# Optimization experiments

Measured on AMD Instinct MI355X. Metric: run time of the kernel, lower is better.

## Reference

```python
import jax, jax.numpy as jnp
import numpy as np

NUM_HEADS = 32
HEAD_DIM = 128
HIDDEN = NUM_HEADS * HEAD_DIM  # 4096
ROPE_BASE = 10000.0
VISION_TOKEN_TYPE = 1


def vision_expert_mask(token_type_ids):
    # vision_token_mask[:, :-1] = (tt[:, :-1]==1) & (tt[:, 1:]==1); last col False
    tt = token_type_ids
    m = (tt[:, :-1] == VISION_TOKEN_TYPE) & (tt[:, 1:] == VISION_TOKEN_TYPE)
    return jnp.concatenate([m, jnp.zeros((tt.shape[0], 1), dtype=bool)], axis=1)


def rotary_cos_sin(position_ids, head_dim, dtype):
    inv_freq = 1.0 / (ROPE_BASE ** (jnp.arange(0, head_dim, 2, dtype=jnp.float32) / head_dim))
    freqs = position_ids.astype(jnp.float32)[..., None] * inv_freq  # [B,S,Dh/2]
    emb = jnp.concatenate([freqs, freqs], axis=-1)  # [B,S,Dh]
    return jnp.cos(emb).astype(dtype), jnp.sin(emb).astype(dtype)


def rotate_half(x):
    d = x.shape[-1] // 2
    return jnp.concatenate([-x[..., d:], x[..., :d]], axis=-1)


def setup_inputs() -> dict:
    key = jax.random.key(0)
    ks = jax.random.split(key, 5)
    B, S = 2, 2048
    hidden_states = jax.random.normal(ks[0], (B, S, HIDDEN), dtype=jnp.float32)
    token_type_ids = jax.random.randint(ks[1], (B, S), 0, 2, dtype=jnp.int64)
    position_ids = jnp.broadcast_to(jnp.arange(S, dtype=jnp.int64)[None, :], (B, S))
    scale = 0.02
    w_vis_qkv = jax.random.normal(ks[2], (HIDDEN, 3 * HIDDEN), dtype=jnp.float32) * scale
    w_lang_qkv = jax.random.normal(ks[3], (HIDDEN, 3 * HIDDEN), dtype=jnp.float32) * scale
    w_vis_dense = jax.random.normal(ks[4], (HIDDEN, HIDDEN), dtype=jnp.float32) * scale
    w_lang_dense = jax.random.normal(jax.random.fold_in(key, 7), (HIDDEN, HIDDEN), dtype=jnp.float32) * scale
    return dict(hidden_states=hidden_states, token_type_ids=token_type_ids,
                position_ids=position_ids, w_vis_qkv=w_vis_qkv, w_lang_qkv=w_lang_qkv,
                w_vis_dense=w_vis_dense, w_lang_dense=w_lang_dense)


def reference(hidden_states, token_type_ids, position_ids,
              w_vis_qkv, w_lang_qkv, w_vis_dense, w_lang_dense):
    B, S, D = hidden_states.shape
    vm = vision_expert_mask(token_type_ids)  # [B,S] bool

    # 2-expert QKV dispatch (mask-select between the two expert GEMMs)
    qkv = jnp.where(vm[..., None],
                    hidden_states @ w_vis_qkv,
                    hidden_states @ w_lang_qkv)  # [B,S,3D]
    q, k, v = jnp.split(qkv, 3, axis=-1)
    q = q.reshape(B, S, NUM_HEADS, HEAD_DIM)
    k = k.reshape(B, S, NUM_HEADS, HEAD_DIM)
    v = v.reshape(B, S, NUM_HEADS, HEAD_DIM)

    # rotary embedding on q, k
    cos, sin = rotary_cos_sin(position_ids, HEAD_DIM, q.dtype)  # [B,S,Dh]
    cos, sin = cos[:, :, None, :], sin[:, :, None, :]
    q = q * cos + rotate_half(q) * sin
    k = k * cos + rotate_half(k) * sin

    # causal attention (dense equivalent of the paged-attention call)
    scores = jnp.einsum('bqhd,bkhd->bhqk', q, k) / jnp.sqrt(jnp.array(HEAD_DIM, q.dtype))
    causal = jnp.tril(jnp.ones((S, S), dtype=bool))
    scores = jnp.where(causal[None, None], scores, jnp.finfo(scores.dtype).min)
    probs = jax.nn.softmax(scores, axis=-1)
    ctx = jnp.einsum('bhqk,bkhd->bqhd', probs, v).reshape(B, S, D)

    # 2-expert output dense dispatch
    attn_output = jnp.where(vm[..., None],
                            ctx @ w_vis_dense,
                            ctx @ w_lang_dense)
    return attn_output
```

## Files before the change

kernel.cpp:

```cpp
#include <hip/hip_runtime.h>
#include <math.h>

#define SEQ     2048
#define NB      2
#define NHEADS  32
#define DHEAD   128
#define HID     4096
#define NQKV    12288
#define T_TOKENS (NB*SEQ)

typedef _Float16 half8 __attribute__((ext_vector_type(8)));
typedef float v4f __attribute__((ext_vector_type(4)));

__device__ __forceinline__ void gload_lds16(const void* g, void* l) {
    __builtin_amdgcn_global_load_lds(
        (__attribute__((address_space(1))) void*)(void*)(g),
        (__attribute__((address_space(3))) void*)(unsigned)(unsigned long long)(l),
        16, 0, 0);
}

__device__ __forceinline__ v4f mfma16(half8 a, half8 b, v4f c) {
    return __builtin_amdgcn_mfma_f32_16x16x32_f16(a, b, c, 0, 0, 0);
}

__global__ void route_kernel(const int* __restrict__ tt, int* counts, int* idx) {
    int t = blockIdx.x * blockDim.x + threadIdx.x;
    if (t >= T_TOKENS) return;
    int s = t & (SEQ - 1);
    bool vm = (s < SEQ - 1) && (tt[t] == 1) && (tt[t + 1] == 1);
    int e = vm ? 0 : 1;
    int p = atomicAdd(&counts[e], 1);
    idx[e * T_TOKENS + p] = t;
}

__global__ void rope_table_kernel(const int* __restrict__ pos_ids, float2* __restrict__ tab) {
    int i = blockIdx.x * blockDim.x + threadIdx.x;
    if (i >= T_TOKENS * 64) return;
    int tok = i >> 6, j = i & 63;
    float invf = (float)pow(10000.0, -(double)j * (1.0 / 64.0));
    float ang = (float)pos_ids[tok] * invf;
    double ds, dc;
    sincos((double)ang, &ds, &dc);
    tab[i] = make_float2((float)dc, (float)ds);
}

__global__ void cvt_f32_f16(const float* __restrict__ src, _Float16* __restrict__ dst, int n4) {
    int i = blockIdx.x * blockDim.x + threadIdx.x;
    if (i >= n4) return;
    float4 v = ((const float4*)src)[i];
    union { _Float16 h[4]; uint2 u; } p;
    p.h[0] = (_Float16)v.x; p.h[1] = (_Float16)v.y;
    p.h[2] = (_Float16)v.z; p.h[3] = (_Float16)v.w;
    ((uint2*)dst)[i] = p.u;
}

__global__ void transpose_cvt(const float* __restrict__ W, _Float16* __restrict__ WT,
                              int K, int N) {
    __shared__ _Float16 t[64][72];
    const int n0 = blockIdx.x * 64, k0 = blockIdx.y * 64;
    const int cr = threadIdx.x & 15, rr = threadIdx.x >> 4;
#pragma unroll
    for (int it = 0; it < 4; ++it) {
        int r = rr + it * 16;
        float4 v = *(const float4*)&W[(size_t)(k0 + r) * N + n0 + cr * 4];
        t[cr*4+0][r] = (_Float16)v.x; t[cr*4+1][r] = (_Float16)v.y;
        t[cr*4+2][r] = (_Float16)v.z; t[cr*4+3][r] = (_Float16)v.w;
    }
    __syncthreads();
#pragma unroll
    for (int it = 0; it < 4; ++it) {
        int r = rr + it * 16;
        union { _Float16 h[4]; uint2 u; } p;
#pragma unroll
        for (int j = 0; j < 4; ++j) p.h[j] = t[r][cr*4+j];
        *(uint2*)&WT[(size_t)(n0 + r) * K + k0 + cr * 4] = p.u;
    }
}

__global__ void transpose_v(const _Float16* __restrict__ vin, _Float16* __restrict__ vout) {
    __shared__ _Float16 t[64][72];
    const int s0 = blockIdx.x * 64;
    const int d0 = blockIdx.y * 64;
    const int bh = blockIdx.z;
    const int b = bh >> 5, h = bh & 31;
    const int cr = threadIdx.x & 15, rr = threadIdx.x >> 4;
#pragma unroll
    for (int it = 0; it < 4; ++it) {
        int sl = rr + it * 16;
        union { _Float16 h4[4]; uint2 u; } p;
        p.u = *(const uint2*)&vin[(size_t)(b * SEQ + s0 + sl) * HID + h * DHEAD + d0 + cr * 4];
#pragma unroll
        for (int j = 0; j < 4; ++j) t[cr*4+j][sl] = p.h4[j];
    }
    __syncthreads();
#pragma unroll
    for (int it = 0; it < 4; ++it) {
        int dl = rr + it * 16;
        union { _Float16 h4[4]; uint2 u; } p;
#pragma unroll
        for (int j = 0; j < 4; ++j) p.h4[j] = t[dl][cr*4+j];
        *(uint2*)&vout[((size_t)bh * DHEAD + d0 + dl) * SEQ + s0 + cr * 4] = p.u;
    }
}

template <int MODE, int NCT>
__global__ __launch_bounds__(256, 2)
void gemm_expert(const _Float16* __restrict__ A,
                 const _Float16* __restrict__ BT0,
                 const _Float16* __restrict__ BT1,
                 const int* __restrict__ counts,
                 const int* __restrict__ idx_all,
                 const float2* __restrict__ rope,
                 _Float16* __restrict__ qbuf,
                 _Float16* __restrict__ kbuf,
                 _Float16* __restrict__ vbuf,
                 float* __restrict__ out) {
    const int e = blockIdx.z;
    const int count = counts[e];

    const int f   = blockIdx.x + NCT * blockIdx.y;
    const int xcd = f & 7;
    const int g   = f >> 3;
    const int c   = g >> 6;
    const int wi  = g & 63;
    const int rt  = wi >> 1;
    const int ct  = xcd * (NCT / 8) + c * 2 + (wi & 1);

    if (rt * 128 >= count) return;
    const int* idx = idx_all + e * T_TOKENS;
    const _Float16* BT = e ? BT1 : BT0;

    __shared__ _Float16 sA[2][128 * 32];
    __shared__ _Float16 sB[2][128 * 32];

    const int tid = threadIdx.x;
    const int w = tid >> 6, lane = tid & 63;
    const int col = lane & 15, quad = lane >> 4;

    const int r0 = (w * 2 + 0) * 16 + (lane >> 2);
    const int r1 = (w * 2 + 1) * 16 + (lane >> 2);
    int g0 = rt * 128 + r0; if (g0 > count - 1) g0 = count - 1;
    int g1 = rt * 128 + r1; if (g1 > count - 1) g1 = count - 1;
    const int tok0 = idx[g0], tok1 = idx[g1];
    const _Float16* ag0 = A + (size_t)tok0 * HID + (lane & 3) * 8;
    const _Float16* ag1 = A + (size_t)tok1 * HID + (lane & 3) * 8;
    const _Float16* bg0 = BT + (size_t)(ct * 128 + r0) * HID + (lane & 3) * 8;
    const _Float16* bg1 = BT + (size_t)(ct * 128 + r1) * HID + (lane & 3) * 8;
    const int sa_off0 = (w * 2 + 0) * 512;
    const int sa_off1 = (w * 2 + 1) * 512;

    v4f acc[2][8];
#pragma unroll
    for (int i = 0; i < 2; ++i)
#pragma unroll
        for (int j = 0; j < 8; ++j) { v4f z = {0.f, 0.f, 0.f, 0.f}; acc[i][j] = z; }

    const int am0 = (w * 32 + col) * 32 + quad * 8;
    const int am1 = am0 + 16 * 32;

    gload_lds16(ag0, &sA[0][sa_off0]); gload_lds16(ag1, &sA[0][sa_off1]);
    gload_lds16(bg0, &sB[0][sa_off0]); gload_lds16(bg1, &sB[0][sa_off1]);
    ag0 += 32; ag1 += 32; bg0 += 32; bg1 += 32;
    __syncthreads();

    for (int kt = 0; kt < HID / 32; ++kt) {
        const int cur = kt & 1, nxt = cur ^ 1;
        if (kt + 1 < HID / 32) {
            gload_lds16(ag0, &sA[nxt][sa_off0]); gload_lds16(ag1, &sA[nxt][sa_off1]);
            gload_lds16(bg0, &sB[nxt][sa_off0]); gload_lds16(bg1, &sB[nxt][sa_off1]);
            ag0 += 32; ag1 += 32; bg0 += 32; bg1 += 32;
        }
        half8 a0 = *(const half8*)&sA[cur][am0];
        half8 a1 = *(const half8*)&sA[cur][am1];
#pragma unroll
        for (int nt = 0; nt < 8; ++nt) {
            half8 b = *(const half8*)&sB[cur][(nt * 16 + col) * 32 + quad * 8];
            acc[0][nt] = mfma16(a0, b, acc[0][nt]);
            acc[1][nt] = mfma16(a1, b, acc[1][nt]);
        }
        __syncthreads();
    }

    const int n0 = ct * 128;
    if (MODE == 1) {
#pragma unroll
        for (int mt = 0; mt < 2; ++mt)
#pragma unroll
            for (int r = 0; r < 4; ++r) {
                int rg = rt * 128 + w * 32 + mt * 16 + quad * 4 + r;
                if (rg >= count) continue;
                int tok = idx[rg];
                float* dst = out + (size_t)tok * HID + n0;
#pragma unroll
                for (int nt = 0; nt < 8; ++nt) dst[nt * 16 + col] = acc[mt][nt][r];
            }
    } else {
        const int sec = n0 >> 12;
        const int h = (n0 >> 7) & 31;
#pragma unroll
        for (int mt = 0; mt < 2; ++mt)
#pragma unroll
            for (int r = 0; r < 4; ++r) {
                int rg = rt * 128 + w * 32 + mt * 16 + quad * 4 + r;
                if (rg >= count) continue;
                int tok = idx[rg];
                int b = tok >> 11, s = tok & (SEQ - 1);
                if (sec == 2) {
                    _Float16* dst = vbuf + (size_t)tok * HID + h * DHEAD;
#pragma unroll
                    for (int nt = 0; nt < 8; ++nt) dst[nt * 16 + col] = (_Float16)acc[mt][nt][r];
                } else {
                    _Float16* dst = (sec ? kbuf : qbuf) + ((size_t)(b * NHEADS + h) * SEQ + s) * DHEAD;
                    const float2* tp = rope + (size_t)tok * 64;
#pragma unroll
                    for (int nt = 0; nt < 4; ++nt) {
                        int d = nt * 16 + col;
                        float2 cs = tp[d];
                        float x = acc[mt][nt][r], y = acc[mt][nt + 4][r];
                        dst[d]      = (_Float16)(x * cs.x - y * cs.y);
                        dst[d + 64] = (_Float16)(y * cs.x + x * cs.y);
                    }
                }
            }
    }
}

__global__ __launch_bounds__(256, 2)
void attn_kernel(const _Float16* __restrict__ qbuf,
                 const _Float16* __restrict__ kbuf,
                 const _Float16* __restrict__ vt,
                 _Float16* __restrict__ ctx) {
    const int f   = blockIdx.x;
    const int xcd = f & 7;
    const int t   = f >> 3;
    const int s   = t & 31;
    const int rr  = t >> 5;
    const int u   = s & 15, g = s >> 4;
    const int bh  = xcd * 8 + rr * 2 + g;
    const int qt  = (rr & 1) ? (15 - u) : u;

    const int b = bh >> 5, h = bh & 31;
    const int tid = threadIdx.x;
    const int w = tid >> 6, lane = tid & 63;
    const int col = lane & 15, quad = lane >> 4;

    __shared__ _Float16 sK[2][64 * 128];
    __shared__ _Float16 sV[2][128 * 64];
    __shared__ _Float16 sP[128 * 64];

    half8 qf[2][4];
    const _Float16 qscale = (_Float16)0.08838834764831845f;
#pragma unroll
    for (int mt = 0; mt < 2; ++mt)
#pragma unroll
        for (int kc = 0; kc < 4; ++kc) {
            int row = qt * 128 + w * 32 + mt * 16 + col;
            half8 v = *(const half8*)&qbuf[((size_t)bh * SEQ + row) * DHEAD + kc * 32 + quad * 8];
            qf[mt][kc] = v * qscale;
        }

    float mrow[2][4], lrow[2][4];
    v4f o[2][8];
#pragma unroll
    for (int mt = 0; mt < 2; ++mt)
#pragma unroll
        for (int r = 0; r < 4; ++r) { mrow[mt][r] = -3.0e38f; lrow[mt][r] = 0.f; }
#pragma unroll
    for (int i = 0; i < 2; ++i)
#pragma unroll
        for (int j = 0; j < 8; ++j) { v4f z = {0.f, 0.f, 0.f, 0.f}; o[i][j] = z; }

    const int cxor = col & 7;
    const int vs_chk = (lane & 7) ^ (lane >> 3);
    const int nkt = 2 * qt + 2;

    const _Float16* kg0 = kbuf + (size_t)bh * SEQ * DHEAD;
    const _Float16* vg0 = vt + (size_t)bh * DHEAD * SEQ;

    auto stage = [&](int kt, int buf) {
        const _Float16* kg = kg0 + (size_t)kt * 64 * DHEAD;
        const _Float16* vg = vg0 + kt * 64;
#pragma unroll
        for (int op = 0; op < 4; ++op) {
            int r0 = (w * 4 + op) * 4;
            int krow = r0 + quad;
            int kcs = col ^ (krow & 7);
            gload_lds16(kg + (size_t)krow * DHEAD + kcs * 8, &sK[buf][r0 * 128]);
            int d0 = (w * 4 + op) * 8;
            int vrow = d0 + (lane >> 3);
            gload_lds16(vg + (size_t)vrow * SEQ + vs_chk * 8, &sV[buf][d0 * 64]);
        }
    };

    stage(0, 0);
    __syncthreads();

    for (int kt = 0; kt < nkt; ++kt) {
        const int cur = kt & 1;
        if (kt + 1 < nkt) stage(kt + 1, cur ^ 1);

        v4f sc[2][4];
#pragma unroll
        for (int i = 0; i < 2; ++i)
#pragma unroll
            for (int j = 0; j < 4; ++j) { v4f z = {0.f, 0.f, 0.f, 0.f}; sc[i][j] = z; }
#pragma unroll
        for (int kc = 0; kc < 4; ++kc) {
            const int kof = ((kc * 4 + quad) ^ cxor) * 8;
#pragma unroll
            for (int nt = 0; nt < 4; ++nt) {
                half8 bf = *(const half8*)&sK[cur][(size_t)(nt * 16 + col) * 128 + kof];
                sc[0][nt] = mfma16(qf[0][kc], bf, sc[0][nt]);
                sc[1][nt] = mfma16(qf[1][kc], bf, sc[1][nt]);
            }
        }

        if (kt >= 2 * qt) {
#pragma unroll
            for (int mt = 0; mt < 2; ++mt)
#pragma unroll
                for (int nt = 0; nt < 4; ++nt)
#pragma unroll
                    for (int r = 0; r < 4; ++r) {
                        int rowa = qt * 128 + w * 32 + mt * 16 + quad * 4 + r;
                        int cola = kt * 64 + nt * 16 + col;
                        if (cola > rowa) sc[mt][nt][r] = -3.0e38f;
                    }
        }

#pragma unroll
        for (int mt = 0; mt < 2; ++mt)
#pragma unroll
            for (int r = 0; r < 4; ++r) {
                float mx = sc[mt][0][r];
#pragma unroll
                for (int nt = 1; nt < 4; ++nt) mx = fmaxf(mx, sc[mt][nt][r]);
                mx = fmaxf(mx, __shfl_xor(mx, 1));
                mx = fmaxf(mx, __shfl_xor(mx, 2));
                mx = fmaxf(mx, __shfl_xor(mx, 4));
                mx = fmaxf(mx, __shfl_xor(mx, 8));
                float newm = fmaxf(mrow[mt][r], mx);
                float alpha = __expf(mrow[mt][r] - newm);
                mrow[mt][r] = newm;
                float rs = 0.f;
#pragma unroll
                for (int nt = 0; nt < 4; ++nt) {
                    float p = __expf(sc[mt][nt][r] - newm);
                    sc[mt][nt][r] = p;
                    rs += p;
                }
                rs += __shfl_xor(rs, 1); rs += __shfl_xor(rs, 2);
                rs += __shfl_xor(rs, 4); rs += __shfl_xor(rs, 8);
                lrow[mt][r] = lrow[mt][r] * alpha + rs;
#pragma unroll
                for (int nt = 0; nt < 8; ++nt) o[mt][nt][r] *= alpha;
            }

#pragma unroll
        for (int mt = 0; mt < 2; ++mt)
#pragma unroll
            for (int nt = 0; nt < 4; ++nt)
#pragma unroll
                for (int r = 0; r < 4; ++r) {
                    int rp = w * 32 + mt * 16 + quad * 4 + r;
                    int colh = nt * 16 + col;
                    int c = (colh >> 3) ^ (rp & 7);
                    sP[(size_t)rp * 64 + c * 8 + (colh & 7)] = (_Float16)sc[mt][nt][r];
                }

#pragma unroll
        for (int kc = 0; kc < 2; ++kc) {
            const int kof = ((kc * 4 + quad) ^ cxor) * 8;
            half8 p0 = *(const half8*)&sP[(size_t)(w * 32 + col) * 64 + kof];
            half8 p1 = *(const half8*)&sP[(size_t)(w * 32 + 16 + col) * 64 + kof];
#pragma unroll
            for (int nt = 0; nt < 8; ++nt) {
                half8 vf = *(const half8*)&sV[cur][(size_t)(nt * 16 + col) * 64 + kof];
                o[0][nt] = mfma16(p0, vf, o[0][nt]);
                o[1][nt] = mfma16(p1, vf, o[1][nt]);
            }
        }

        __syncthreads();
    }

#pragma unroll
    for (int mt = 0; mt < 2; ++mt)
#pragma unroll
        for (int r = 0; r < 4; ++r) {
            int rowa = qt * 128 + w * 32 + mt * 16 + quad * 4 + r;
            float inv = 1.0f / lrow[mt][r];
            _Float16* dst = ctx + ((size_t)b * SEQ + rowa) * HID + h * DHEAD;
#pragma unroll
            for (int nt = 0; nt < 8; ++nt)
                dst[nt * 16 + col] = (_Float16)(o[mt][nt][r] * inv);
        }
}

extern "C" void kernel_launch(void* const* d_in, const int* in_sizes, int n_in,
                              void* d_out, int out_size, void* d_ws, size_t ws_size,
                              hipStream_t stream) {
    const float* hidden = (const float*)d_in[0];
    const int*   tt     = (const int*)d_in[1];
    const int*   pos    = (const int*)d_in[2];
    const float* wvq    = (const float*)d_in[3];
    const float* wlq    = (const float*)d_in[4];
    const float* wvd    = (const float*)d_in[5];
    const float* wld    = (const float*)d_in[6];
    float* out = (float*)d_out;

    char* ws = (char*)d_ws;
    size_t off = 0;
    auto alloc = [&](size_t bytes) {
        char* p = ws + off;
        off += (bytes + 255) & ~(size_t)255;
        return p;
    };
    const size_t TOKB = (size_t)T_TOKENS * HID * sizeof(_Float16);
    _Float16* h16  = (_Float16*)alloc(TOKB);
    _Float16* wvqT = (_Float16*)alloc((size_t)NQKV * HID * 2);
    _Float16* wlqT = (_Float16*)alloc((size_t)NQKV * HID * 2);
    _Float16* wvdT = (_Float16*)alloc((size_t)HID * HID * 2);
    _Float16* wldT = (_Float16*)alloc((size_t)HID * HID * 2);
    _Float16* qb   = (_Float16*)alloc(TOKB);
    _Float16* kb   = (_Float16*)alloc(TOKB);
    _Float16* vtmp = (_Float16*)alloc(TOKB);
    int* counts = (int*)alloc(2 * sizeof(int));
    int* idx    = (int*)alloc(2 * T_TOKENS * sizeof(int));
    float2* rope = (float2*)alloc((size_t)T_TOKENS * 64 * sizeof(float2));
    _Float16* vT  = h16;
    _Float16* ctx = vtmp;

    hipMemsetAsync(counts, 0, 2 * sizeof(int), stream);
    route_kernel<<<T_TOKENS / 256, 256, 0, stream>>>(tt, counts, idx);
    rope_table_kernel<<<(T_TOKENS * 64) / 256, 256, 0, stream>>>(pos, rope);
    cvt_f32_f16<<<(T_TOKENS * HID / 4) / 256, 256, 0, stream>>>(hidden, h16, T_TOKENS * HID / 4);
    transpose_cvt<<<dim3(NQKV / 64, HID / 64), 256, 0, stream>>>(wvq, wvqT, HID, NQKV);
    transpose_cvt<<<dim3(NQKV / 64, HID / 64), 256, 0, stream>>>(wlq, wlqT, HID, NQKV);
    transpose_cvt<<<dim3(HID / 64, HID / 64), 256, 0, stream>>>(wvd, wvdT, HID, HID);
    transpose_cvt<<<dim3(HID / 64, HID / 64), 256, 0, stream>>>(wld, wldT, HID, HID);
    gemm_expert<0, NQKV / 128><<<dim3(NQKV / 128, T_TOKENS / 128, 2), 256, 0, stream>>>(
        h16, wvqT, wlqT, counts, idx, rope, qb, kb, vtmp, nullptr);
    transpose_v<<<dim3(SEQ / 64, DHEAD / 64, NB * NHEADS), 256, 0, stream>>>(vtmp, vT);
    attn_kernel<<<dim3(16 * NB * NHEADS), 256, 0, stream>>>(qb, kb, vT, ctx);
    gemm_expert<1, HID / 128><<<dim3(HID / 128, T_TOKENS / 128, 2), 256, 0, stream>>>(
        ctx, wvdT, wldT, counts, idx, nullptr, nullptr, nullptr, nullptr, out);
}
```

Measured before the change: 1.613 ms.

## Deepen GEMM LDS pipeline to four stages with explicit vmcnt waits

Turns the expert GEMM's double-buffered LDS staging into a 4-buffer ring that keeps three tiles of async global-to-LDS loads in flight. Each step waits with s_waitcnt vmcnt and a single barrier, then issues the next stage and computes the current one. The goal is to hide global load latency better and drop one barrier per iteration. In exchange LDS use doubles to 64KB per block, which may lower occupancy, and correctness now depends on the hand-counted vmcnt values.

Measured after the change: 1.553 ms. 1.04x faster.

```diff
diff --git a/kernel.cpp b/kernel.cpp
--- a/kernel.cpp
+++ b/kernel.cpp
@@ -130,8 +130,8 @@
     const int* idx = idx_all + e * T_TOKENS;
     const _Float16* BT = e ? BT1 : BT0;
 
-    __shared__ _Float16 sA[2][128 * 32];
-    __shared__ _Float16 sB[2][128 * 32];
+    __shared__ _Float16 sA[4][128 * 32];
+    __shared__ _Float16 sB[4][128 * 32];
 
     const int tid = threadIdx.x;
     const int w = tid >> 6, lane = tid & 63;
@@ -158,18 +158,12 @@
     const int am0 = (w * 32 + col) * 32 + quad * 8;
     const int am1 = am0 + 16 * 32;
 
-    gload_lds16(ag0, &sA[0][sa_off0]); gload_lds16(ag1, &sA[0][sa_off1]);
-    gload_lds16(bg0, &sB[0][sa_off0]); gload_lds16(bg1, &sB[0][sa_off1]);
-    ag0 += 32; ag1 += 32; bg0 += 32; bg1 += 32;
-    __syncthreads();
-
-    for (int kt = 0; kt < HID / 32; ++kt) {
-        const int cur = kt & 1, nxt = cur ^ 1;
-        if (kt + 1 < HID / 32) {
-            gload_lds16(ag0, &sA[nxt][sa_off0]); gload_lds16(ag1, &sA[nxt][sa_off1]);
-            gload_lds16(bg0, &sB[nxt][sa_off0]); gload_lds16(bg1, &sB[nxt][sa_off1]);
-            ag0 += 32; ag1 += 32; bg0 += 32; bg1 += 32;
-        }
+    auto stage = [&](int buf) {
+        gload_lds16(ag0, &sA[buf][sa_off0]); gload_lds16(ag1, &sA[buf][sa_off1]);
+        gload_lds16(bg0, &sB[buf][sa_off0]); gload_lds16(bg1, &sB[buf][sa_off1]);
+        ag0 += 32; ag1 += 32; bg0 += 32; bg1 += 32;
+    };
+    auto compute = [&](int cur) {
         half8 a0 = *(const half8*)&sA[cur][am0];
         half8 a1 = *(const half8*)&sA[cur][am1];
 #pragma unroll
@@ -178,8 +172,30 @@
             acc[0][nt] = mfma16(a0, b, acc[0][nt]);
             acc[1][nt] = mfma16(a1, b, acc[1][nt]);
         }
-        __syncthreads();
-    }
+    };
+
+    const int NK = HID / 32;
+    stage(0); stage(1); stage(2);
+
+    for (int kt = 0; kt < NK - 3; ++kt) {
+        asm volatile("s_waitcnt vmcnt(8)" ::: "memory");
+        __builtin_amdgcn_s_barrier();
+        asm volatile("" ::: "memory");
+        stage((kt + 3) & 3);
+        compute(kt & 3);
+    }
+    asm volatile("s_waitcnt vmcnt(8)" ::: "memory");
+    __builtin_amdgcn_s_barrier();
+    asm volatile("" ::: "memory");
+    compute((NK - 3) & 3);
+    asm volatile("s_waitcnt vmcnt(4)" ::: "memory");
+    __builtin_amdgcn_s_barrier();
+    asm volatile("" ::: "memory");
+    compute((NK - 2) & 3);
+    asm volatile("s_waitcnt vmcnt(0)" ::: "memory");
+    __builtin_amdgcn_s_barrier();
+    asm volatile("" ::: "memory");
+    compute((NK - 1) & 3);
 
     const int n0 = ct * 128;
     if (MODE == 1) {
```
